# Kernel optimization log

Measured on AMD Instinct MI355X. Metric: run time of the kernel, lower is better.

## Reference

```python
import jax, jax.numpy as jnp
import numpy as np

B, N, C, K = 16, 2000, 4, 8
EPS = 1e-5


def setup_inputs() -> dict:
    key = jax.random.key(0)
    ks = jax.random.split(key, 10)
    def p(k, shape, s=0.1):
        return jax.random.normal(k, shape, jnp.float32) * s
    return {
        "data": jax.random.normal(ks[0], (B, 1, N, C), jnp.float32),
        "x": jax.random.normal(ks[1], (B, 1, N, 4), jnp.float32),
        "w1a": p(ks[2], (128, C)), "b1a": jnp.zeros((128,), jnp.float32),
        "w1b": p(ks[3], (128, 128)), "b1b": jnp.zeros((128,), jnp.float32),
        "w2": p(ks[4], (128, 2 * C + 2)), "b2": jnp.zeros((128,), jnp.float32),
        "res_wa": p(ks[5], (4, 128, 128)), "res_ba": jnp.zeros((4, 128), jnp.float32),
        "res_wb": p(ks[6], (4, 128, 128)), "res_bb": jnp.zeros((4, 128), jnp.float32),
        "wl": p(ks[7], (1, 128)), "bl": jnp.zeros((1,), jnp.float32),
    }


def conv1x1(t, w, b):
    # t: [B, Cin, H, W], w: [Cout, Cin]
    return jnp.einsum('bchw,oc->bohw', t, w) + b[None, :, None, None]


def bn(t):
    # training-mode BatchNorm2d, gamma=1 beta=0 (default init)
    m = jnp.mean(t, axis=(0, 2, 3), keepdims=True)
    v = jnp.var(t, axis=(0, 2, 3), keepdims=True)
    return (t - m) * jax.lax.rsqrt(v + EPS)


def instn(t):
    # InstanceNorm2d, affine=False
    m = jnp.mean(t, axis=(2, 3), keepdims=True)
    v = jnp.var(t, axis=(2, 3), keepdims=True)
    return (t - m) * jax.lax.rsqrt(v + EPS)


def res_block(t, wa, ba, wb, bb):
    h = jax.nn.relu(bn(instn(conv1x1(t, wa, ba))))
    h = bn(instn(conv1x1(h, wb, bb)))
    return jax.nn.relu(h + t)


def knn_idx(f, k):
    # f: [B, D, N]; negative squared distance, top-(k+1), drop self
    xx = jnp.sum(f * f, axis=1)                        # [B, N]
    inner = jnp.einsum('bdn,bdm->bnm', f, f)           # [B, N, N]
    pd = 2.0 * inner - xx[:, :, None] - xx[:, None, :]
    idx = jax.lax.top_k(pd, k + 1)[1]                  # [B, N, k+1]
    return idx[:, :, 1:]


def graph_feature(f, idx):
    # f: [B, D, N], idx: [B, N, k] -> [B, 2D, N, k]
    xf = jnp.transpose(f, (0, 2, 1))                   # [B, N, D]
    nb = jax.vmap(lambda a, i: a[i])(xf, idx)          # [B, N, k, D]
    xt = xf[:, :, None, :]
    gf = jnp.concatenate([jnp.broadcast_to(xt, nb.shape), xt - nb], axis=-1)
    return jnp.transpose(gf, (0, 3, 1, 2))


def reference(data, x, w1a, b1a, w1b, b1b, w2, b2,
              res_wa, res_ba, res_wb, res_bb, wl, bl):
    n = data.shape[2]
    t = jnp.transpose(data, (0, 3, 2, 1))              # [B, C, N, 1]

    # self_attention
    h = conv1x1(t, w1a, b1a)
    h = jax.nn.relu(bn(h))
    h = conv1x1(h, w1b, b1b)[..., 0]                   # [B, 128, N]
    h = h / (jnp.linalg.norm(h, axis=1, keepdims=True) + 1e-5)
    A_rowsum = jnp.einsum('bcn,bcm->bm', h, h)         # sum_i A[i, j]
    D = (A_rowsum - 1.0) / n                           # [B, N] (eye subtraction)
    feat = jnp.concatenate(
        [t, jax.nn.relu(jnp.tanh(D))[:, None, :, None]], axis=1)  # [B, C+1, N, 1]

    f = feat[..., 0]                                   # [B, C+1, N]
    idx = knn_idx(f, K)
    g = graph_feature(f, idx)                          # [B, 2C+2, N, K]

    out = jax.nn.relu(bn(conv1x1(g, w2, b2)))          # [B, 128, N, K]
    out = jnp.max(out, axis=-1, keepdims=True)         # [B, 128, N, 1]

    for i in range(4):
        out = res_block(out, res_wa[i], res_ba[i], res_wb[i], res_bb[i])

    logit = conv1x1(out, wl, bl)[:, 0, :, 0]           # [B, N]

    # weighted 8-point
    weights = jax.nn.relu(jnp.tanh(logit))             # [B, N]
    xp = jnp.transpose(x[:, 0], (0, 2, 1))             # [B, 4, N]
    ones = jnp.ones_like(xp[:, 0])
    X = jnp.stack([xp[:, 2] * xp[:, 0], xp[:, 2] * xp[:, 1], xp[:, 2],
                   xp[:, 3] * xp[:, 0], xp[:, 3] * xp[:, 1], xp[:, 3],
                   xp[:, 0], xp[:, 1], ones], axis=1)  # [B, 9, N]
    X = jnp.transpose(X, (0, 2, 1))                    # [B, N, 9]
    XwX = jnp.einsum('bnp,bnq->bpq', X, weights[:, :, None] * X)  # [B, 9, 9]
    _, v = jnp.linalg.eigh(XwX)                        # ascending eigvals
    e_hat = v[:, :, 0]                                 # smallest-eig eigenvector
    e_hat = e_hat / jnp.linalg.norm(e_hat, axis=1, keepdims=True)

    return (D, logit, e_hat)
```

## Files before the change

### kernel.cpp

```cpp
#include <hip/hip_runtime.h>
#include <math.h>

#define BB 16
#define NN 2000
#define CH 128
#define KNN 8
#define JCH 8
#define JSZ 250

__device__ inline float wred(float v) {
    for (int off = 32; off > 0; off >>= 1) v += __shfl_down(v, off, 64);
    return v;
}

__global__ void k_conv1(const float* __restrict__ data, const float* __restrict__ w1a,
                        const float* __restrict__ b1a, float* __restrict__ c1) {
    int i = blockIdx.x * 256 + threadIdx.x;
    if (i >= BB * CH * NN) return;
    int n = i % NN;
    int rest = i / NN;
    int o = rest & 127;
    int b = rest >> 7;
    const float* dp = data + (b * NN + n) * 4;
    float acc = b1a[o];
    for (int c = 0; c < 4; ++c) acc += w1a[o * 4 + c] * dp[c];
    c1[i] = acc;
}

__global__ void k_chanstats(const float* __restrict__ src, float* __restrict__ chAB) {
    int o = blockIdx.x;
    int tid = threadIdx.x;
    float s = 0.f, ss = 0.f;
    for (int b = 0; b < BB; ++b) {
        const float* p = src + (b * CH + o) * NN;
        for (int n = tid; n < NN; n += 256) { float v = p[n]; s += v; ss += v * v; }
    }
    s = wred(s); ss = wred(ss);
    __shared__ float sh[8];
    int wid = tid >> 6, lane = tid & 63;
    if (lane == 0) { sh[wid] = s; sh[4 + wid] = ss; }
    __syncthreads();
    if (tid == 0) {
        float S0 = sh[0] + sh[1] + sh[2] + sh[3];
        float SS = sh[4] + sh[5] + sh[6] + sh[7];
        float m = S0 / (float)(BB * NN);
        float var = SS / (float)(BB * NN) - m * m;
        float a = rsqrtf(var + 1e-5f);
        chAB[o] = a;
        chAB[CH + o] = -m * a;
    }
}

__global__ __launch_bounds__(256) void k_gemm(const float* __restrict__ X, const float* __restrict__ W,
                                              const float* __restrict__ bias, float* __restrict__ Y,
                                              const float* __restrict__ ab, int mode) {
    int ot = blockIdx.x, by = blockIdx.y;
    int b = by >> 5, nt = by & 31;
    int n0 = nt * 64, o0 = ot * 64;
    int tid = threadIdx.x;
    int tx = tid & 15, ty = tid >> 4;
    __shared__ float Xs[32][64];
    __shared__ float Ws[32][68];
    float acc[4][4] = {};
    for (int jc = 0; jc < 4; ++jc) {
        for (int q = 0; q < 8; ++q) {
            int e = q * 256 + tid;
            int jj = e >> 6, nn = e & 63;
            int j = jc * 32 + jj, n = n0 + nn;
            float v = 0.f;
            if (n < NN) {
                v = X[(b * CH + j) * NN + n];
                if (mode == 1) v = fmaxf(ab[j] * v + ab[CH + j], 0.f);
                else if (mode == 2) { int bc = b * CH + j; v = fmaxf(ab[bc * 2] * v + ab[bc * 2 + 1], 0.f); }
            }
            Xs[jj][nn] = v;
        }
        for (int q = 0; q < 8; ++q) {
            int e = q * 256 + tid;
            int jj = e & 31, oo = e >> 5;
            Ws[jj][oo] = W[(o0 + oo) * CH + jc * 32 + jj];
        }
        __syncthreads();
        for (int jj = 0; jj < 32; ++jj) {
            float4 wv = *(const float4*)&Ws[jj][ty * 4];
            float4 xv = *(const float4*)&Xs[jj][tx * 4];
            float wva[4] = {wv.x, wv.y, wv.z, wv.w};
            float xva[4] = {xv.x, xv.y, xv.z, xv.w};
#pragma unroll
            for (int a = 0; a < 4; ++a)
#pragma unroll
                for (int bq = 0; bq < 4; ++bq) acc[a][bq] += wva[a] * xva[bq];
        }
        __syncthreads();
    }
    for (int a = 0; a < 4; ++a) {
        int o = o0 + ty * 4 + a;
        float bi = bias[o];
        for (int q = 0; q < 4; ++q) {
            int n = n0 + tx * 4 + q;
            if (n < NN) Y[(b * CH + o) * NN + n] = acc[a][q] + bi;
        }
    }
}

__global__ void k_invn(const float* __restrict__ h2, float* __restrict__ invn) {
    int b = blockIdx.x >> 3, chunk = blockIdx.x & 7;
    int n = chunk * 256 + threadIdx.x;
    if (n >= NN) return;
    float acc = 0.f;
    for (int c = 0; c < CH; ++c) { float v = h2[(b * CH + c) * NN + n]; acc += v * v; }
    invn[b * NN + n] = 1.f / (sqrtf(acc) + 1e-5f);
}

__global__ void k_S(const float* __restrict__ h2, const float* __restrict__ invn, float* __restrict__ Sv) {
    int row = blockIdx.x;
    int b = row >> 7;
    const float* p = h2 + row * NN;
    const float* iv = invn + b * NN;
    float s = 0.f;
    for (int n = threadIdx.x; n < NN; n += 256) s += p[n] * iv[n];
    s = wred(s);
    __shared__ float sh[4];
    int wid = threadIdx.x >> 6, lane = threadIdx.x & 63;
    if (lane == 0) sh[wid] = s;
    __syncthreads();
    if (threadIdx.x == 0) Sv[row] = sh[0] + sh[1] + sh[2] + sh[3];
}

__global__ void k_Df(const float* __restrict__ h2, const float* __restrict__ invn,
                     const float* __restrict__ Sv, const float* __restrict__ data,
                     float* __restrict__ outD, float* __restrict__ f5) {
    int b = blockIdx.x >> 3, chunk = blockIdx.x & 7;
    int n = chunk * 256 + threadIdx.x;
    if (n >= NN) return;
    float acc = 0.f;
    for (int c = 0; c < CH; ++c) acc += h2[(b * CH + c) * NN + n] * Sv[b * CH + c];
    float Ar = acc * invn[b * NN + n];
    float Dv = (Ar - 1.0f) / (float)NN;
    outD[b * NN + n] = Dv;
    const float* dp = data + (b * NN + n) * 4;
    for (int c = 0; c < 4; ++c) f5[(b * 5 + c) * NN + n] = dp[c];
    f5[(b * 5 + 4) * NN + n] = fmaxf(tanhf(Dv), 0.f);
}

__global__ __launch_bounds__(256) void k_knn_part(const float* __restrict__ f5,
                                                  float* __restrict__ pd, int* __restrict__ pj) {
    __shared__ float4 fs4[JSZ];
    __shared__ float fs1[JSZ];
    int jc = blockIdx.x, ic = blockIdx.y, b = blockIdx.z;
    int j0 = jc * JSZ;
    int tid = threadIdx.x;
    const float* fb = f5 + b * 5 * NN;
    for (int e = tid; e < JSZ; e += 256) {
        float4 v;
        v.x = fb[0 * NN + j0 + e];
        v.y = fb[1 * NN + j0 + e];
        v.z = fb[2 * NN + j0 + e];
        v.w = fb[3 * NN + j0 + e];
        fs4[e] = v;
        fs1[e] = fb[4 * NN + j0 + e];
    }
    __syncthreads();
    int i = ic * 256 + tid;
    if (i >= NN) return;
    float fi0 = fb[i], fi1 = fb[NN + i], fi2 = fb[2 * NN + i], fi3 = fb[3 * NN + i], fi4 = fb[4 * NN + i];
    float bd[8]; int bj[8];
#pragma unroll
    for (int q = 0; q < 8; ++q) { bd[q] = 1e30f; bj[q] = 0x7fffffff; }
    auto ins = [&](float cd, int cj) {
#pragma unroll
        for (int q = 0; q < 8; ++q) {
            bool lt = cd < bd[q];
            float td = lt ? bd[q] : cd;
            int tj = lt ? bj[q] : cj;
            bd[q] = lt ? cd : bd[q];
            bj[q] = lt ? cj : bj[q];
            cd = td; cj = tj;
        }
    };
    for (int jj = 0; jj < JSZ; jj += 2) {
        float4 fja = fs4[jj];
        float fa4 = fs1[jj];
        float4 fjb = fs4[jj + 1];
        float fb4 = fs1[jj + 1];
        float a0 = fi0 - fja.x, a1 = fi1 - fja.y, a2 = fi2 - fja.z, a3 = fi3 - fja.w, a4 = fi4 - fa4;
        float da = a0 * a0 + a1 * a1 + a2 * a2 + a3 * a3 + a4 * a4;
        float b0 = fi0 - fjb.x, b1 = fi1 - fjb.y, b2 = fi2 - fjb.z, b3 = fi3 - fjb.w, b4 = fi4 - fb4;
        float db = b0 * b0 + b1 * b1 + b2 * b2 + b3 * b3 + b4 * b4;
        int ja = j0 + jj, jb = j0 + jj + 1;
        if (ja != i && da < bd[7]) ins(da, ja);
        if (jb != i && db < bd[7]) ins(db, jb);
    }
    long base = ((long)(b * NN + i) * JCH + jc) * 8;
#pragma unroll
    for (int q = 0; q < 8; ++q) { pd[base + q] = bd[q]; pj[base + q] = bj[q]; }
}

__global__ __launch_bounds__(256) void k_knn_merge(const float* __restrict__ pd, const int* __restrict__ pj,
                                                   int* __restrict__ idxb) {
    int s = blockIdx.x * 256 + threadIdx.x;
    if (s >= BB * NN) return;
    const float* dl = pd + (long)s * JCH * 8;
    const int* jl = pj + (long)s * JCH * 8;
    int ptr[JCH];
#pragma unroll
    for (int c = 0; c < JCH; ++c) ptr[c] = 0;
    for (int q = 0; q < 8; ++q) {
        float best = 1e38f; int bestj = 0x7fffffff; int bc = 0;
#pragma unroll
        for (int c = 0; c < JCH; ++c) {
            if (ptr[c] < 8) {
                float d = dl[c * 8 + ptr[c]];
                int j = jl[c * 8 + ptr[c]];
                if (d < best || (d == best && j < bestj)) { best = d; bestj = j; bc = c; }
            }
        }
        idxb[s * 8 + q] = bestj;
        ++ptr[bc];
    }
}

__global__ __launch_bounds__(256) void k_gstats(const float* __restrict__ f5, const int* __restrict__ idxb,
                                                double* __restrict__ gacc) {
    int s = blockIdx.x * 256 + threadIdx.x;
    float acc[65];
#pragma unroll
    for (int q = 0; q < 65; ++q) acc[q] = 0.f;
    if (s < BB * NN) {
        int b = s / NN, n = s - b * NN;
        float fo[5];
#pragma unroll
        for (int c = 0; c < 5; ++c) fo[c] = f5[(b * 5 + c) * NN + n];
        float sd[5] = {0, 0, 0, 0, 0};
        float sdd[15];
#pragma unroll
        for (int q = 0; q < 15; ++q) sdd[q] = 0.f;
        for (int k = 0; k < 8; ++k) {
            int j = idxb[s * 8 + k];
            float df[5];
#pragma unroll
            for (int c = 0; c < 5; ++c) df[c] = fo[c] - f5[(b * 5 + c) * NN + j];
#pragma unroll
            for (int c = 0; c < 5; ++c) sd[c] += df[c];
            int t = 0;
#pragma unroll
            for (int c = 0; c < 5; ++c)
#pragma unroll
                for (int d2 = c; d2 < 5; ++d2) { sdd[t] += df[c] * df[d2]; ++t; }
        }
#pragma unroll
        for (int c = 0; c < 5; ++c) { acc[c] = 8.f * fo[c]; acc[5 + c] = sd[c]; }
        int t = 10, sc = 0;
        for (int p = 0; p < 10; ++p)
            for (int q = p; q < 10; ++q) {
                float v;
                if (q < 5) v = 8.f * fo[p] * fo[q];
                else if (p < 5) v = fo[p] * sd[q - 5];
                else { v = sdd[sc]; ++sc; }
                acc[t++] = v;
            }
    }
#pragma unroll 1
    for (int q = 0; q < 65; ++q) {
        float v = acc[q];
        for (int off = 32; off > 0; off >>= 1) v += __shfl_down(v, off, 64);
        acc[q] = v;
    }
    __shared__ float sh[4][65];
    int lane = threadIdx.x & 63, wid = threadIdx.x >> 6;
    if (lane == 0) {
        for (int q = 0; q < 65; ++q) sh[wid][q] = acc[q];
    }
    __syncthreads();
    if (threadIdx.x < 65) {
        float tot = sh[0][threadIdx.x] + sh[1][threadIdx.x] + sh[2][threadIdx.x] + sh[3][threadIdx.x];
        atomicAdd(&gacc[threadIdx.x], (double)tot);
    }
}

__global__ void k_gfinal(const double* __restrict__ gacc, const float* __restrict__ w2,
                         const float* __restrict__ b2, float* __restrict__ g2ab) {
    int o = threadIdx.x;
    if (o >= 128) return;
    double inv = 1.0 / (double)(BB * NN * 8);
    double Wr[10];
    for (int c = 0; c < 10; ++c) Wr[c] = (double)w2[o * 10 + c];
    double gm[10];
    for (int c = 0; c < 10; ++c) gm[c] = gacc[c] * inv;
    double b0 = (double)b2[o];
    double mean = b0;
    for (int c = 0; c < 10; ++c) mean += Wr[c] * gm[c];
    double e2 = b0 * b0 + 2.0 * b0 * (mean - b0);
    int t = 10;
    for (int p = 0; p < 10; ++p)
        for (int q = p; q < 10; ++q) {
            double G = gacc[t] * inv; ++t;
            double contrib = Wr[p] * Wr[q] * G;
            e2 += (p == q) ? contrib : 2.0 * contrib;
        }
    double var = e2 - mean * mean;
    double a = 1.0 / sqrt(var + 1e-5);
    g2ab[o] = (float)a;
    g2ab[128 + o] = (float)(-mean * a);
}

__global__ __launch_bounds__(256) void k_graphconv(const float* __restrict__ f5, const int* __restrict__ idxb,
                                                   const float* __restrict__ w2, const float* __restrict__ b2,
                                                   const float* __restrict__ g2ab, float* __restrict__ x0) {
    __shared__ float ws[1280], bs[128];
    __shared__ float fo_s[16][5], fnb_s[16][8][5];
    __shared__ int idxs[16][8];
    int b = blockIdx.x / 125, tile = blockIdx.x % 125;
    int nbase = tile * 16;
    int tid = threadIdx.x;
    for (int e = tid; e < 1280; e += 256) ws[e] = w2[e];
    if (tid < 128) bs[tid] = b2[tid];
    if (tid < 128) { int nn = tid >> 3, k = tid & 7; idxs[nn][k] = idxb[(b * NN + nbase + nn) * 8 + k]; }
    if (tid >= 128 && tid < 208) { int e = tid - 128; int nn = e / 5, c = e % 5; fo_s[nn][c] = f5[(b * 5 + c) * NN + nbase + nn]; }
    __syncthreads();
    for (int e = tid; e < 640; e += 256) {
        int nn = e / 40, r = e % 40, k = r / 5, c = r % 5;
        fnb_s[nn][k][c] = f5[(b * 5 + c) * NN + idxs[nn][k]];
    }
    __syncthreads();
    int nn = tid & 15, og = tid >> 4;
    float fo[5];
#pragma unroll
    for (int c = 0; c < 5; ++c) fo[c] = fo_s[nn][c];
    for (int oo = 0; oo < 8; ++oo) {
        int o = og * 8 + oo;
        float base = bs[o];
        float wn[5];
#pragma unroll
        for (int c = 0; c < 5; ++c) {
            float w1 = ws[o * 10 + c], w5 = ws[o * 10 + 5 + c];
            base += (w1 + w5) * fo[c];
            wn[c] = w5;
        }
        float mx = -1e30f;
        for (int k = 0; k < 8; ++k) {
            float v = base;
#pragma unroll
            for (int c = 0; c < 5; ++c) v -= wn[c] * fnb_s[nn][k][c];
            mx = fmaxf(mx, v);
        }
        float y = fmaxf(g2ab[o] * mx + g2ab[128 + o], 0.f);
        x0[(b * CH + o) * NN + nbase + nn] = y;
    }
}

__global__ void k_rowstats(const float* __restrict__ src, float* __restrict__ stats) {
    int row = blockIdx.x;
    const float* p = src + row * NN;
    float s = 0.f, ss = 0.f;
    for (int n = threadIdx.x; n < NN; n += 256) { float v = p[n]; s += v; ss += v * v; }
    s = wred(s); ss = wred(ss);
    __shared__ float sh[8];
    int wid = threadIdx.x >> 6, lane = threadIdx.x & 63;
    if (lane == 0) { sh[wid] = s; sh[4 + wid] = ss; }
    __syncthreads();
    if (threadIdx.x == 0) {
        float S0 = sh[0] + sh[1] + sh[2] + sh[3];
        float SS = sh[4] + sh[5] + sh[6] + sh[7];
        float m = S0 / (float)NN;
        float var = SS / (float)NN - m * m;
        stats[row * 2] = m;
        stats[row * 2 + 1] = var;
    }
}

__global__ void k_finalize(const float* __restrict__ stats, float* __restrict__ ab) {
    int c = threadIdx.x;
    if (c >= 128) return;
    float acc = 0.f;
    for (int b = 0; b < BB; ++b) { float var = stats[(b * CH + c) * 2 + 1]; acc += var / (var + 1e-5f); }
    float vc = acc / (float)BB;
    float sc = rsqrtf(vc + 1e-5f);
    for (int b = 0; b < BB; ++b) {
        float m = stats[(b * CH + c) * 2];
        float var = stats[(b * CH + c) * 2 + 1];
        float a = rsqrtf(var + 1e-5f) * sc;
        ab[(b * CH + c) * 2] = a;
        ab[(b * CH + c) * 2 + 1] = -m * a;
    }
}

__global__ void k_resadd(const float* __restrict__ Bm, const float* __restrict__ ab,
                         const float* __restrict__ x, float* __restrict__ y) {
    int i = blockIdx.x * 256 + threadIdx.x;
    if (i >= BB * CH * NN) return;
    int bc = i / NN;
    float v = ab[bc * 2] * Bm[i] + ab[bc * 2 + 1] + x[i];
    y[i] = fmaxf(v, 0.f);
}

__global__ void k_logit(const float* __restrict__ x4, const float* __restrict__ wl,
                        const float* __restrict__ bl, float* __restrict__ outLogit) {
    int b = blockIdx.x >> 3, chunk = blockIdx.x & 7;
    int n = chunk * 256 + threadIdx.x;
    if (n >= NN) return;
    float acc = 0.f;
    for (int c = 0; c < CH; ++c) acc += wl[c] * x4[(b * CH + c) * NN + n];
    outLogit[b * NN + n] = acc + bl[0];
}

__global__ __launch_bounds__(256) void k_xwx(const float* __restrict__ logit, const float* __restrict__ x_in,
                                             float* __restrict__ XwX) {
    int b = blockIdx.x;
    int tid = threadIdx.x;
    float a[45];
#pragma unroll
    for (int q = 0; q < 45; ++q) a[q] = 0.f;
    for (int n = tid; n < NN; n += 256) {
        float lg = logit[b * NN + n];
        float w = fmaxf(tanhf(lg), 0.f);
        const float* xp = x_in + (b * NN + n) * 4;
        float px = xp[0], py = xp[1], z = xp[2], wq = xp[3];
        float X9[9] = {z * px, z * py, z, wq * px, wq * py, wq, px, py, 1.f};
        int t = 0;
#pragma unroll
        for (int p = 0; p < 9; ++p) {
            float wp = w * X9[p];
#pragma unroll
            for (int q = p; q < 9; ++q) { a[t] += wp * X9[q]; ++t; }
        }
    }
#pragma unroll 1
    for (int q = 0; q < 45; ++q) {
        float v = a[q];
        for (int off = 32; off > 0; off >>= 1) v += __shfl_down(v, off, 64);
        a[q] = v;
    }
    __shared__ float sh[4][45];
    int lane = tid & 63, wid = tid >> 6;
    if (lane == 0) {
        for (int q = 0; q < 45; ++q) sh[wid][q] = a[q];
    }
    __syncthreads();
    if (tid < 45) XwX[b * 45 + tid] = sh[0][tid] + sh[1][tid] + sh[2][tid] + sh[3][tid];
}

__device__ __forceinline__ float lgetf(float reg, int i) {
    return __int_as_float(__builtin_amdgcn_readlane(__float_as_int(reg), i));
}
__device__ __forceinline__ float wsum64(float v) {
    for (int off = 32; off > 0; off >>= 1) v += __shfl_xor(v, off, 64);
    return v;
}

__device__ inline float slapy2_f(float x, float y) {
    float xa = fabsf(x), ya = fabsf(y);
    float w = fmaxf(xa, ya), z = fminf(xa, ya);
    if (z == 0.f) return w;
    float q = z / w;
    return w * sqrtf(1.f + q * q);
}

__device__ inline void slartg_f(float f, float g, float& c, float& s, float& r) {
    if (g == 0.f) { c = 1.f; s = 0.f; r = f; }
    else if (f == 0.f) { c = 0.f; s = (g > 0.f ? 1.f : -1.f); r = fabsf(g); }
    else {
        float d = sqrtf(f * f + g * g);
        c = fabsf(f) / d;
        r = (f >= 0.f) ? d : -d;
        s = g / r;
    }
}

__device__ void slaev2_f(float a, float b, float c, float& rt1, float& rt2, float& cs1, float& sn1) {
    float sm = a + c, df = a - c;
    float adf = fabsf(df), tb = b + b, ab = fabsf(tb);
    float acmx, acmn;
    if (fabsf(a) > fabsf(c)) { acmx = a; acmn = c; } else { acmx = c; acmn = a; }
    float rt;
    if (adf > ab) { float q = ab / adf; rt = adf * sqrtf(1.f + q * q); }
    else if (adf < ab) { float q = adf / ab; rt = ab * sqrtf(1.f + q * q); }
    else rt = ab * sqrtf(2.f);
    int sgn1;
    if (sm < 0.f) { rt1 = 0.5f * (sm - rt); sgn1 = -1; rt2 = (acmx / rt1) * acmn - (b / rt1) * b; }
    else if (sm > 0.f) { rt1 = 0.5f * (sm + rt); sgn1 = 1; rt2 = (acmx / rt1) * acmn - (b / rt1) * b; }
    else { rt1 = 0.5f * rt; rt2 = -0.5f * rt; sgn1 = 1; }
    float cs; int sgn2;
    if (df >= 0.f) { cs = df + rt; sgn2 = 1; } else { cs = df - rt; sgn2 = -1; }
    float acs = fabsf(cs);
    if (acs > ab) {
        float ct = -tb / cs;
        sn1 = 1.f / sqrtf(1.f + ct * ct);
        cs1 = ct * sn1;
    } else {
        if (ab == 0.f) { cs1 = 1.f; sn1 = 0.f; }
        else { float tn = -cs / tb; cs1 = 1.f / sqrtf(1.f + tn * tn); sn1 = tn * cs1; }
    }
    if (sgn1 == sgn2) { float tn = cs1; cs1 = -sn1; sn1 = tn; }
}

#define ROTLOG_MAX 2560

__global__ __launch_bounds__(64) void k_eigh(const float* __restrict__ XwX, float* __restrict__ out_e) {
    __shared__ float Am[81];
    __shared__ float rcl[ROTLOG_MAX], rsl[ROTLOG_MAX];
    __shared__ int rjl[ROTLOG_MAX];
    int bb = blockIdx.x;
    int lane = threadIdx.x;
#define AA(i, j) Am[(i) * 9 + (j)]
#define DGET(i) lgetf(dreg, (i))
#define DSET(i, v) do { float _v = (v); dreg = (lane == (i)) ? _v : dreg; } while (0)
#define EGET(i) lgetf(ereg, (i))
#define ESET(i, v) do { float _v = (v); ereg = (lane == (i)) ? _v : ereg; } while (0)
    {
        const float* src = XwX + bb * 45;
        for (int e2 = lane; e2 < 81; e2 += 64) {
            int r0 = e2 / 9, c0 = e2 % 9;
            int a0 = r0 < c0 ? r0 : c0, b0 = r0 < c0 ? c0 : r0;
            int t = a0 * 9 - (a0 * (a0 - 1)) / 2 + (b0 - a0);
            Am[e2] = src[t];
        }
    }
    __syncthreads();
    float dreg = 0.f, ereg = 0.f, treg = 0.f;
    int cnt = 0;
    for (int i = 0; i < 8; ++i) {
        float alpha = AA(i + 1, i);
        float xn2 = 0.f;
        for (int j = i + 2; j < 9; ++j) xn2 += AA(j, i) * AA(j, i);
        float taui;
        if (xn2 == 0.f) { taui = 0.f; ESET(i, alpha); }
        else {
            float xnorm = sqrtf(xn2);
            float beta = slapy2_f(alpha, xnorm);
            beta = (alpha >= 0.f) ? -beta : beta;
            taui = (beta - alpha) / beta;
            float scl = 1.f / (alpha - beta);
            for (int j = i + 2; j < 9; ++j) AA(j, i) *= scl;
            ESET(i, beta);
            float p[9], w[9];
            for (int j = i + 1; j < 9; ++j) {
                float acc = AA(j, i + 1);
                for (int k2 = i + 2; k2 < 9; ++k2) acc += AA(j, k2) * AA(k2, i);
                p[j] = taui * acc;
            }
            float dot = p[i + 1];
            for (int j = i + 2; j < 9; ++j) dot += p[j] * AA(j, i);
            float alpha2 = -0.5f * taui * dot;
            w[i + 1] = p[i + 1] + alpha2;
            for (int j = i + 2; j < 9; ++j) w[j] = p[j] + alpha2 * AA(j, i);
            for (int j = i + 1; j < 9; ++j) {
                float vj = (j == i + 1) ? 1.f : AA(j, i);
                for (int k2 = i + 1; k2 < 9; ++k2) {
                    float vk = (k2 == i + 1) ? 1.f : AA(k2, i);
                    float upd = AA(j, k2) - (vj * w[k2] + w[j] * vk);
                    __syncthreads();
                    if (lane == 0) AA(j, k2) = upd;
                    __syncthreads();
                }
            }
        }
        treg = (lane == i) ? taui : treg;
    }
    dreg = (lane < 9) ? Am[lane * 10] : 0.f;
    const float eps = 5.9604645e-08f;
    const float eps2 = 3.5527137e-15f;
    const float safmin = 1.17549435e-38f;
    const int n = 9;
    int nmaxit = n * 30, jtot = 0;
    int l1 = 0;
    while (l1 <= n - 1) {
        if (l1 > 0) ESET(l1 - 1, 0.f);
        int m = n - 1;
        for (int mm = l1; mm <= n - 2; ++mm) {
            float tst = fabsf(EGET(mm));
            if (tst == 0.f) { m = mm; break; }
            if (tst <= (sqrtf(fabsf(DGET(mm))) * sqrtf(fabsf(DGET(mm + 1)))) * eps) { ESET(mm, 0.f); m = mm; break; }
        }
        int l = l1, lsv = l, lend = m, lendsv = lend;
        l1 = m + 1;
        if (lend == l) continue;
        if (fabsf(DGET(lend)) < fabsf(DGET(l))) { lend = lsv; l = lendsv; }
        if (lend > l) {
            for (;;) {
                int m2 = lend;
                if (l != lend) {
                    for (int mm = l; mm <= lend - 1; ++mm) {
                        float em = EGET(mm);
                        float tst = em * em;
                        if (tst <= (eps2 * fabsf(DGET(mm))) * fabsf(DGET(mm + 1)) + safmin) { m2 = mm; break; }
                    }
                }
                if (m2 < lend) ESET(m2, 0.f);
                float p = DGET(l);
                if (m2 == l) { DSET(l, p); ++l; if (l <= lend) continue; else break; }
                if (m2 == l + 1) {
                    float rt1, rt2, c, s;
                    slaev2_f(DGET(l), EGET(l), DGET(l + 1), rt1, rt2, c, s);
                    if (lane == 0) { rcl[cnt] = c; rsl[cnt] = s; rjl[cnt] = l; }
                    ++cnt;
                    DSET(l, rt1); DSET(l + 1, rt2); ESET(l, 0.f); l += 2;
                    if (l <= lend) continue; else break;
                }
                if (jtot == nmaxit) break;
                ++jtot;
                float g = (DGET(l + 1) - p) / (2.f * EGET(l));
                float r = slapy2_f(g, 1.f);
                g = DGET(m2) - p + EGET(l) / (g + (g >= 0.f ? fabsf(r) : -fabsf(r)));
                float s = 1.f, c = 1.f;
                p = 0.f;
                for (int i = m2 - 1; i >= l; --i) {
                    float ei = EGET(i);
                    float f = s * ei, bq = c * ei;
                    slartg_f(g, f, c, s, r);
                    if (i != m2 - 1) ESET(i + 1, r);
                    g = DGET(i + 1) - p;
                    r = (DGET(i) - g) * s + 2.f * c * bq;
                    p = s * r;
                    DSET(i + 1, g + p);
                    g = c * r - bq;
                    if (lane == 0) { rcl[cnt] = c; rsl[cnt] = -s; rjl[cnt] = i; }
                    ++cnt;
                }
                DSET(l, DGET(l) - p);
                ESET(l, g);
            }
        } else {
            for (;;) {
                int m2 = lend;
                if (l != lend) {
                    for (int mm = l; mm >= lend + 1; --mm) {
                        float em = EGET(mm - 1);
                        float tst = em * em;
                        if (tst <= (eps2 * fabsf(DGET(mm))) * fabsf(DGET(mm - 1)) + safmin) { m2 = mm; break; }
                    }
                }
                if (m2 > lend) ESET(m2 - 1, 0.f);
                float p = DGET(l);
                if (m2 == l) { DSET(l, p); --l; if (l >= lend) continue; else break; }
                if (m2 == l - 1) {
                    float rt1, rt2, c, s;
                    slaev2_f(DGET(l - 1), EGET(l - 1), DGET(l), rt1, rt2, c, s);
                    if (lane == 0) { rcl[cnt] = c; rsl[cnt] = s; rjl[cnt] = l - 1; }
                    ++cnt;
                    DSET(l - 1, rt1); DSET(l, rt2); ESET(l - 1, 0.f); l -= 2;
                    if (l >= lend) continue; else break;
                }
                if (jtot == nmaxit) break;
                ++jtot;
                float g = (DGET(l - 1) - p) / (2.f * EGET(l - 1));
                float r = slapy2_f(g, 1.f);
                g = DGET(m2) - p + EGET(l - 1) / (g + (g >= 0.f ? fabsf(r) : -fabsf(r)));
                float s = 1.f, c = 1.f;
                p = 0.f;
                for (int i = m2; i <= l - 1; ++i) {
                    float ei = EGET(i);
                    float f = s * ei, bq = c * ei;
                    slartg_f(g, f, c, s, r);
                    if (i != m2) ESET(i - 1, r);
                    g = DGET(i) - p;
                    r = (DGET(i + 1) - g) * s + 2.f * c * bq;
                    p = s * r;
                    DSET(i, g + p);
                    g = c * r - bq;
                    if (lane == 0) { rcl[cnt] = c; rsl[cnt] = s; rjl[cnt] = i; }
                    ++cnt;
                }
                DSET(l, DGET(l) - p);
                ESET(l - 1, g);
            }
        }
    }
    __syncthreads();
    int permreg = lane;
    for (int ii = 1; ii < 9; ++ii) {
        int i = ii - 1, kk = i;
        float p = DGET(i);
        for (int j = ii; j < 9; ++j) {
            float dj = DGET(j);
            if (dj < p) { kk = j; p = dj; }
        }
        if (kk != i) {
            float di = DGET(i);
            DSET(kk, di);
            DSET(i, p);
            int pi = __builtin_amdgcn_readlane(permreg, i);
            int pk = __builtin_amdgcn_readlane(permreg, kk);
            permreg = (lane == i) ? pk : permreg;
            permreg = (lane == kk) ? pi : permreg;
        }
    }
    int kcol = __builtin_amdgcn_readlane(permreg, 0);
    float v0reg = (lane == kcol) ? 1.f : 0.f;
    for (int t = cnt - 1; t >= 0; --t) {
        float c = rcl[t], s = rsl[t];
        int j = rjl[t];
        float a = lgetf(v0reg, j);
        float b2 = lgetf(v0reg, j + 1);
        float nj = c * a - s * b2;
        float nj1 = s * a + c * b2;
        v0reg = (lane == j) ? nj : v0reg;
        v0reg = (lane == j + 1) ? nj1 : v0reg;
    }
    for (int i = 7; i >= 0; --i) {
        float ti = lgetf(treg, i);
        if (ti == 0.f) continue;
        float avi = (lane >= i + 2 && lane <= 8) ? Am[lane * 9 + i] : 0.f;
        float contrib = 0.f;
        if (lane == i + 1) contrib = v0reg;
        else if (lane >= i + 2 && lane <= 8) contrib = avi * v0reg;
        float dot = wsum64(contrib) * ti;
        if (lane == i + 1) v0reg -= dot;
        else if (lane >= i + 2 && lane <= 8) v0reg -= avi * dot;
    }
    float sq = (lane < 9) ? v0reg * v0reg : 0.f;
    float nrm = sqrtf(wsum64(sq));
    if (lane < 9) out_e[bb * 9 + lane] = v0reg / nrm;
#undef AA
#undef DGET
#undef DSET
#undef EGET
#undef ESET
}

extern "C" void kernel_launch(void* const* d_in, const int* in_sizes, int n_in,
                              void* d_out, int out_size, void* d_ws, size_t ws_size,
                              hipStream_t stream) {
    const float* data = (const float*)d_in[0];
    const float* x_in = (const float*)d_in[1];
    const float* w1a = (const float*)d_in[2];
    const float* b1a = (const float*)d_in[3];
    const float* w1b = (const float*)d_in[4];
    const float* b1b = (const float*)d_in[5];
    const float* w2 = (const float*)d_in[6];
    const float* b2 = (const float*)d_in[7];
    const float* res_wa = (const float*)d_in[8];
    const float* res_ba = (const float*)d_in[9];
    const float* res_wb = (const float*)d_in[10];
    const float* res_bb = (const float*)d_in[11];
    const float* wl = (const float*)d_in[12];
    const float* bl = (const float*)d_in[13];
    float* out = (float*)d_out;

    double* gacc = (double*)d_ws;
    float* xwx = (float*)((char*)d_ws + 1024);
    float* fbase = (float*)((char*)d_ws + 16384);
    float* big0 = fbase;
    float* big1 = big0 + BB * CH * NN;
    float* big2 = big1 + BB * CH * NN;
    float* tbuf = big2 + BB * CH * NN;
    float* f5 = tbuf + BB * 4 * NN;
    float* invn = f5 + BB * 5 * NN;
    float* Sv = invn + BB * NN;
    int* idxb = (int*)(Sv + BB * CH);
    float* chAB = (float*)(idxb + BB * NN * 8);
    float* stA = chAB + 256;
    float* abA = stA + BB * CH * 2;
    float* stB = abA + BB * CH * 2;
    float* abB = stB + BB * CH * 2;
    float* g2ab = abB + BB * CH * 2;
    float* knn_pd = big2;
    int* knn_pj = (int*)(big2 + BB * NN * JCH * 8);

    hipMemsetAsync(d_ws, 0, 1024, stream);

    k_conv1<<<16000, 256, 0, stream>>>(data, w1a, b1a, big0);
    k_chanstats<<<128, 256, 0, stream>>>(big0, chAB);
    k_gemm<<<dim3(2, 512), 256, 0, stream>>>(big0, w1b, b1b, big1, chAB, 1);
    k_invn<<<128, 256, 0, stream>>>(big1, invn);
    k_S<<<2048, 256, 0, stream>>>(big1, invn, Sv);
    k_Df<<<128, 256, 0, stream>>>(big1, invn, Sv, data, out, f5);
    k_knn_part<<<dim3(JCH, 8, BB), 256, 0, stream>>>(f5, knn_pd, knn_pj);
    k_knn_merge<<<125, 256, 0, stream>>>(knn_pd, knn_pj, idxb);
    k_gstats<<<125, 256, 0, stream>>>(f5, idxb, gacc);
    k_gfinal<<<1, 128, 0, stream>>>(gacc, w2, b2, g2ab);
    k_graphconv<<<2000, 256, 0, stream>>>(f5, idxb, w2, b2, g2ab, big0);

    float* xb = big0;
    float* hb = big1;
    for (int i = 0; i < 4; ++i) {
        k_gemm<<<dim3(2, 512), 256, 0, stream>>>(xb, res_wa + i * CH * CH, res_ba + i * CH, hb, nullptr, 0);
        k_rowstats<<<2048, 256, 0, stream>>>(hb, stA);
        k_finalize<<<1, 128, 0, stream>>>(stA, abA);
        k_gemm<<<dim3(2, 512), 256, 0, stream>>>(hb, res_wb + i * CH * CH, res_bb + i * CH, big2, abA, 2);
        k_rowstats<<<2048, 256, 0, stream>>>(big2, stB);
        k_finalize<<<1, 128, 0, stream>>>(stB, abB);
        k_resadd<<<16000, 256, 0, stream>>>(big2, abB, xb, hb);
        float* tmp = xb; xb = hb; hb = tmp;
    }

    k_logit<<<128, 256, 0, stream>>>(xb, wl, bl, out + BB * NN);
    k_xwx<<<16, 256, 0, stream>>>(out + BB * NN, x_in, xwx);
    k_eigh<<<16, 64, 0, stream>>>(xwx, out + 2 * BB * NN);
}
```

Baseline: 818.2 us.

## Replace per-candidate top-8 insertion with batched bitonic sort-merge in kNN

The kNN partial kernel now evaluates candidates in groups of 8, sorts each group with a sorting network, and merges it into the running top-8 via a bitonic merge. This replaces the per-candidate, divergent insertion chain with branch-free compare-and-swaps. The shared tile is padded to 256 entries with large sentinel values, so each thread does a few extra distance computations. Separately, k_gstats moves to 128-thread blocks with twice as many blocks for more parallelism, at the cost of twice as many double atomics.

```diff
diff --git a/kernel.cpp b/kernel.cpp
--- a/kernel.cpp
+++ b/kernel.cpp
@@ -143,22 +143,34 @@
     f5[(b * 5 + 4) * NN + n] = fmaxf(tanhf(Dv), 0.f);
 }
 
+__device__ __forceinline__ void cas_dj(float& da, int& ja, float& db, int& jb) {
+    bool sw = (db < da) || (db == da && jb < ja);
+    float t0 = sw ? db : da;
+    float t1 = sw ? da : db;
+    int u0 = sw ? jb : ja;
+    int u1 = sw ? ja : jb;
+    da = t0; db = t1; ja = u0; jb = u1;
+}
+
 __global__ __launch_bounds__(256) void k_knn_part(const float* __restrict__ f5,
                                                   float* __restrict__ pd, int* __restrict__ pj) {
-    __shared__ float4 fs4[JSZ];
-    __shared__ float fs1[JSZ];
+    __shared__ float4 fs4[256];
+    __shared__ float fs1[256];
     int jc = blockIdx.x, ic = blockIdx.y, b = blockIdx.z;
     int j0 = jc * JSZ;
     int tid = threadIdx.x;
     const float* fb = f5 + b * 5 * NN;
-    for (int e = tid; e < JSZ; e += 256) {
+    if (tid < JSZ) {
         float4 v;
-        v.x = fb[0 * NN + j0 + e];
-        v.y = fb[1 * NN + j0 + e];
-        v.z = fb[2 * NN + j0 + e];
-        v.w = fb[3 * NN + j0 + e];
-        fs4[e] = v;
-        fs1[e] = fb[4 * NN + j0 + e];
+        v.x = fb[0 * NN + j0 + tid];
+        v.y = fb[1 * NN + j0 + tid];
+        v.z = fb[2 * NN + j0 + tid];
+        v.w = fb[3 * NN + j0 + tid];
+        fs4[tid] = v;
+        fs1[tid] = fb[4 * NN + j0 + tid];
+    } else {
+        fs4[tid] = make_float4(1e18f, 1e18f, 1e18f, 1e18f);
+        fs1[tid] = 1e18f;
     }
     __syncthreads();
     int i = ic * 256 + tid;
@@ -167,29 +179,45 @@
     float bd[8]; int bj[8];
 #pragma unroll
     for (int q = 0; q < 8; ++q) { bd[q] = 1e30f; bj[q] = 0x7fffffff; }
-    auto ins = [&](float cd, int cj) {
+    for (int g = 0; g < 256; g += 8) {
+        float d[8]; int jv[8];
+#pragma unroll
+        for (int k = 0; k < 8; ++k) {
+            float4 fj = fs4[g + k];
+            float f4 = fs1[g + k];
+            float a0 = fi0 - fj.x, a1 = fi1 - fj.y, a2 = fi2 - fj.z, a3 = fi3 - fj.w, a4 = fi4 - f4;
+            float dd = a0 * a0 + a1 * a1 + a2 * a2 + a3 * a3 + a4 * a4;
+            int jj = j0 + g + k;
+            d[k] = (jj == i) ? 3.0e38f : dd;
+            jv[k] = jj;
+        }
+        cas_dj(d[0], jv[0], d[1], jv[1]); cas_dj(d[2], jv[2], d[3], jv[3]);
+        cas_dj(d[4], jv[4], d[5], jv[5]); cas_dj(d[6], jv[6], d[7], jv[7]);
+        cas_dj(d[0], jv[0], d[2], jv[2]); cas_dj(d[1], jv[1], d[3], jv[3]);
+        cas_dj(d[4], jv[4], d[6], jv[6]); cas_dj(d[5], jv[5], d[7], jv[7]);
+        cas_dj(d[1], jv[1], d[2], jv[2]); cas_dj(d[5], jv[5], d[6], jv[6]);
+        cas_dj(d[0], jv[0], d[4], jv[4]); cas_dj(d[1], jv[1], d[5], jv[5]);
+        cas_dj(d[2], jv[2], d[6], jv[6]); cas_dj(d[3], jv[3], d[7], jv[7]);
+        cas_dj(d[2], jv[2], d[4], jv[4]); cas_dj(d[3], jv[3], d[5], jv[5]);
+        cas_dj(d[1], jv[1], d[2], jv[2]); cas_dj(d[3], jv[3], d[4], jv[4]);
+        cas_dj(d[5], jv[5], d[6], jv[6]);
+        float nb[8]; int nj[8];
 #pragma unroll
         for (int q = 0; q < 8; ++q) {
-            bool lt = cd < bd[q];
-            float td = lt ? bd[q] : cd;
-            int tj = lt ? bj[q] : cj;
-            bd[q] = lt ? cd : bd[q];
-            bj[q] = lt ? cj : bj[q];
-            cd = td; cj = tj;
-        }
-    };
-    for (int jj = 0; jj < JSZ; jj += 2) {
-        float4 fja = fs4[jj];
-        float fa4 = fs1[jj];
-        float4 fjb = fs4[jj + 1];
-        float fb4 = fs1[jj + 1];
-        float a0 = fi0 - fja.x, a1 = fi1 - fja.y, a2 = fi2 - fja.z, a3 = fi3 - fja.w, a4 = fi4 - fa4;
-        float da = a0 * a0 + a1 * a1 + a2 * a2 + a3 * a3 + a4 * a4;
-        float b0 = fi0 - fjb.x, b1 = fi1 - fjb.y, b2 = fi2 - fjb.z, b3 = fi3 - fjb.w, b4 = fi4 - fb4;
-        float db = b0 * b0 + b1 * b1 + b2 * b2 + b3 * b3 + b4 * b4;
-        int ja = j0 + jj, jb = j0 + jj + 1;
-        if (ja != i && da < bd[7]) ins(da, ja);
-        if (jb != i && db < bd[7]) ins(db, jb);
+            float xd = bd[q]; int xj = bj[q];
+            float yd = d[7 - q]; int yj = jv[7 - q];
+            bool kp = (xd < yd) || (xd == yd && xj < yj);
+            nb[q] = kp ? xd : yd;
+            nj[q] = kp ? xj : yj;
+        }
+        cas_dj(nb[0], nj[0], nb[4], nj[4]); cas_dj(nb[1], nj[1], nb[5], nj[5]);
+        cas_dj(nb[2], nj[2], nb[6], nj[6]); cas_dj(nb[3], nj[3], nb[7], nj[7]);
+        cas_dj(nb[0], nj[0], nb[2], nj[2]); cas_dj(nb[1], nj[1], nb[3], nj[3]);
+        cas_dj(nb[4], nj[4], nb[6], nj[6]); cas_dj(nb[5], nj[5], nb[7], nj[7]);
+        cas_dj(nb[0], nj[0], nb[1], nj[1]); cas_dj(nb[2], nj[2], nb[3], nj[3]);
+        cas_dj(nb[4], nj[4], nb[5], nj[5]); cas_dj(nb[6], nj[6], nb[7], nj[7]);
+#pragma unroll
+        for (int q = 0; q < 8; ++q) { bd[q] = nb[q]; bj[q] = nj[q]; }
     }
     long base = ((long)(b * NN + i) * JCH + jc) * 8;
 #pragma unroll
@@ -220,9 +248,9 @@
     }
 }
 
-__global__ __launch_bounds__(256) void k_gstats(const float* __restrict__ f5, const int* __restrict__ idxb,
+__global__ __launch_bounds__(128) void k_gstats(const float* __restrict__ f5, const int* __restrict__ idxb,
                                                 double* __restrict__ gacc) {
-    int s = blockIdx.x * 256 + threadIdx.x;
+    int s = blockIdx.x * 128 + threadIdx.x;
     float acc[65];
 #pragma unroll
     for (int q = 0; q < 65; ++q) acc[q] = 0.f;
@@ -266,14 +294,14 @@
         for (int off = 32; off > 0; off >>= 1) v += __shfl_down(v, off, 64);
         acc[q] = v;
     }
-    __shared__ float sh[4][65];
+    __shared__ float sh[2][65];
     int lane = threadIdx.x & 63, wid = threadIdx.x >> 6;
     if (lane == 0) {
         for (int q = 0; q < 65; ++q) sh[wid][q] = acc[q];
     }
     __syncthreads();
     if (threadIdx.x < 65) {
-        float tot = sh[0][threadIdx.x] + sh[1][threadIdx.x] + sh[2][threadIdx.x] + sh[3][threadIdx.x];
+        float tot = sh[0][threadIdx.x] + sh[1][threadIdx.x];
         atomicAdd(&gacc[threadIdx.x], (double)tot);
     }
 }
@@ -767,7 +795,7 @@
     k_Df<<<128, 256, 0, stream>>>(big1, invn, Sv, data, out, f5);
     k_knn_part<<<dim3(JCH, 8, BB), 256, 0, stream>>>(f5, knn_pd, knn_pj);
     k_knn_merge<<<125, 256, 0, stream>>>(knn_pd, knn_pj, idxb);
-    k_gstats<<<125, 256, 0, stream>>>(f5, idxb, gacc);
+    k_gstats<<<250, 128, 0, stream>>>(f5, idxb, gacc);
     k_gfinal<<<1, 128, 0, stream>>>(gacc, w2, b2, g2ab);
     k_graphconv<<<2000, 256, 0, stream>>>(f5, idxb, w2, b2, g2ab, big0);
 
```

New measurement: 822.0 us. No clear change (+0.5%).
